# Kernel optimization log

Measured on AMD Instinct MI355X. Metric: run time of the kernel, lower is better.

Reference implementation:

```python
import jax, jax.numpy as jnp
import numpy as np
from jax import lax

K, D = 7, 2                      # kernel_size, dilation
PAD = (K - 1) * D                # = 12, matches init padding
B, CIN, COUT, L = 8, 128, 256, 4096


def _na_indices(L2, k, d):
    """NATTEN-style dilated 1D neighborhood: key positions + rel-pos-bias indices."""
    i = jnp.arange(L2)
    r, ii = i % d, i // d
    Lg = (L2 - r + d - 1) // d                       # dilation-group lengths
    start = jnp.clip(ii - k // 2, 0, Lg - k)         # clamped window start (in-group)
    t = jnp.arange(k)
    pos = r[:, None] + d * (start[:, None] + t[None, :])        # [L2,k] key positions
    bidx = start[:, None] + t[None, :] - ii[:, None] + (k - 1)  # [L2,k] rpb index in [0,2k-2]
    return pos, bidx


def setup_inputs() -> dict:
    key = jax.random.key(0)
    ks = jax.random.split(key, 11)
    s = 0.05
    return {
        "x": jax.random.normal(ks[0], (B, CIN, L), jnp.float32),
        "conv1_v": jax.random.normal(ks[1], (COUT, CIN, K), jnp.float32) * s,
        "conv1_g": jax.random.uniform(ks[2], (COUT,), jnp.float32, 0.5, 1.5),
        "conv1_b": jax.random.normal(ks[3], (COUT,), jnp.float32) * s,
        "qkv_w": jax.random.normal(ks[4], (3 * COUT, COUT), jnp.float32) * s,
        "qkv_b": jax.random.normal(ks[5], (3 * COUT,), jnp.float32) * s,
        "rpb": jax.random.normal(ks[6], (1, 2 * K - 1), jnp.float32) * s,
        "proj_w": jax.random.normal(ks[7], (COUT, COUT), jnp.float32) * s,
        "proj_b": jax.random.normal(ks[8], (COUT,), jnp.float32) * s,
        "ds_w": jax.random.normal(ks[9], (COUT, CIN, 1), jnp.float32) * s,
        "ds_b": jax.random.normal(ks[10], (COUT,), jnp.float32) * s,
    }


def reference(x, conv1_v, conv1_g, conv1_b, qkv_w, qkv_b, rpb, proj_w, proj_b, ds_w, ds_b):
    # weight_norm: w = g * v / ||v|| over (in_ch, kernel) per out channel
    vn = jnp.sqrt(jnp.sum(conv1_v * conv1_v, axis=(1, 2), keepdims=True))
    w1 = conv1_g[:, None, None] * conv1_v / vn
    out = lax.conv_general_dilated(x, w1, (1,), [(PAD, PAD)], rhs_dilation=(D,),
                                   dimension_numbers=("NCH", "OIH", "NCH"))
    out = out + conv1_b[None, :, None]
    out = jax.nn.relu(out[:, :, :-PAD])              # chomp1 + relu (dropout = eval identity)

    # left-pad then neighborhood attention on [B, L2, C]
    h = jnp.pad(out, ((0, 0), (0, 0), (PAD, 0))).transpose(0, 2, 1)
    L2 = h.shape[1]
    qkv = h @ qkv_w.T + qkv_b
    q, k_, v = jnp.split(qkv, 3, axis=-1)            # single head, head_dim = COUT
    pos, bidx = _na_indices(L2, K, D)
    kg = k_[:, pos, :]                               # [B, L2, K, C]
    vg = v[:, pos, :]
    scores = jnp.einsum("blc,blkc->blk", q * (COUT ** -0.5), kg) + rpb[0][bidx][None]
    attn = jax.nn.softmax(scores, axis=-1)
    o = jnp.einsum("blk,blkc->blc", attn, vg) @ proj_w.T + proj_b

    out = jax.nn.relu(o.transpose(0, 2, 1)[:, :, :-PAD])   # chomp2 + relu
    res = jnp.einsum("bcl,oc->bol", x, ds_w[:, :, 0]) + ds_b[None, :, None]
    return jax.nn.relu(out + res)
```

## Files before the change

### kernel.cpp

```cpp
#include <hip/hip_runtime.h>
#include <math.h>

#define KW 7
#define PADW 12
#define BATCH 8
#define CIN 128
#define COUT 256
#define LEN 4096
#define L2V 4108
#define NQKV 768
#define KCONV 896
#define PTILE 64

typedef unsigned short u16;
typedef short v8s __attribute__((ext_vector_type(8)));
typedef float v4f __attribute__((ext_vector_type(4)));

#define KEY3(r) ((((r) & 3) ^ (((r) >> 2) & 1)))

__device__ __forceinline__ u16 f2bf(float f) {
  unsigned int x = __float_as_uint(f);
  x += 0x7fffu + ((x >> 16) & 1u);
  return (u16)(x >> 16);
}
__device__ __forceinline__ float bf2f(u16 u) {
  return __uint_as_float(((unsigned int)u) << 16);
}

__device__ __forceinline__ void gll16(const void* g, void* l) {
  __builtin_amdgcn_global_load_lds(
      (const __attribute__((address_space(1))) void*)g,
      (__attribute__((address_space(3))) void*)l, 16, 0, 0);
}

#define MFMA8(ACC, AA, BB)                                                     \
  { _Pragma("unroll") for (int fi_ = 0; fi_ < 4; ++fi_)                        \
    _Pragma("unroll") for (int fj_ = 0; fj_ < 2; ++fj_)                        \
      ACC[fi_][fj_] = __builtin_amdgcn_mfma_f32_16x16x32_bf16(                 \
          AA[fi_], BB[fj_], ACC[fi_][fj_], 0, 0, 0); }

__global__ __launch_bounds__(256) void prep_wn(
    const float* __restrict__ v, const float* __restrict__ g,
    u16* __restrict__ wt)
{
  const int c = blockIdx.x;
  const float* vo = v + (size_t)c * (CIN * KW);
  float s = 0.f;
  for (int i = threadIdx.x; i < CIN * KW; i += 256) { float t = vo[i]; s += t * t; }
#pragma unroll
  for (int off = 1; off < 64; off <<= 1) s += __shfl_xor(s, off);
  __shared__ float red[4];
  if ((threadIdx.x & 63) == 0) red[threadIdx.x >> 6] = s;
  __syncthreads();
  const float tot = red[0] + red[1] + red[2] + red[3];
  const float scale = g[c] / sqrtf(tot);
  for (int i = threadIdx.x; i < CIN * KW; i += 256) {
    const int ci = i / 7, t = i - ci * 7;
    wt[((size_t)c * KW + t) * CIN + ci] = f2bf(vo[i] * scale);
  }
}

__global__ __launch_bounds__(256) void prep_cast(
    const float* __restrict__ qw, const float* __restrict__ pw,
    const float* __restrict__ dw, u16* __restrict__ qwb,
    u16* __restrict__ pwb, u16* __restrict__ dwb)
{
  const int i4 = (blockIdx.x * 256 + threadIdx.x) * 4;
  const float* src; u16* dst; int off;
  if (i4 < 196608)      { src = qw; dst = qwb; off = i4; }
  else if (i4 < 262144) { src = pw; dst = pwb; off = i4 - 196608; }
  else                  { src = dw; dst = dwb; off = i4 - 262144; }
  const float4 vv = *(const float4*)(src + off);
  *(ushort4*)(dst + off) = make_ushort4(f2bf(vv.x), f2bf(vv.y), f2bf(vv.z), f2bf(vv.w));
}

__global__ __launch_bounds__(256) void zero_fill(
    u16* __restrict__ xT, u16* __restrict__ qkv, const float* __restrict__ qb)
{
  const int idx = blockIdx.x * 256 + threadIdx.x;
  if (idx < BATCH * PADW * CIN) {
    const int b = idx / (PADW * CIN), r = idx - b * (PADW * CIN);
    xT[(size_t)b * L2V * CIN + r] = 0;
  } else {
    const int k = idx - BATCH * PADW * CIN;
    const int b = k / (PADW * NQKV), r2 = k - b * (PADW * NQKV);
    const int row = r2 / NQKV, n = r2 - row * NQKV;
    qkv[((size_t)b * L2V + row) * NQKV + n] = f2bf(qb[n]);
  }
}

__global__ __launch_bounds__(256) void xpose(const float* __restrict__ x, u16* __restrict__ xT)
{
  const int b = blockIdx.y, p0 = blockIdx.x * 64;
  const int tx = threadIdx.x & 15, ty = threadIdx.x >> 4;
  const int p = p0 + ty * 4;
  const float* xb = x + (size_t)b * CIN * LEN;
  u16* xTb = xT + (size_t)b * L2V * CIN + (size_t)(PADW + p) * CIN;
#pragma unroll
  for (int half = 0; half < 2; ++half) {
    const int ci0 = half * 64 + tx * 4;
    float r[4][4];
#pragma unroll
    for (int i = 0; i < 4; ++i)
      *(float4*)r[i] = *(const float4*)(xb + (size_t)(ci0 + i) * LEN + p);
#pragma unroll
    for (int j = 0; j < 4; ++j)
      *(ushort4*)(xTb + (size_t)j * CIN + ci0) =
          make_ushort4(f2bf(r[0][j]), f2bf(r[1][j]), f2bf(r[2][j]), f2bf(r[3][j]));
  }
}

__global__ __launch_bounds__(512, 4) void conv_qkv_fused(
    const u16* __restrict__ wt, const u16* __restrict__ xT,
    const float* __restrict__ c1b, const u16* __restrict__ qwb,
    const float* __restrict__ qb, u16* __restrict__ qkv)
{
  const int b = blockIdx.y;
  const int p0 = blockIdx.x * PTILE;
  const int tid = threadIdx.x;
  const int w = tid >> 6, lane = tid & 63;
  const int l15 = lane & 15, kg = lane >> 4;
  const int wA = w >> 1, wB = w & 1;

  __shared__ u16 hA[PTILE * 256];
  __shared__ u16 sA[2][256 * 32];
  __shared__ u16 sB[2][PTILE * 32];

  const u16* xTb = xT + (size_t)b * L2V * CIN + (size_t)p0 * CIN;

  v4f acc[4][2];
#pragma unroll
  for (int i = 0; i < 4; ++i)
#pragma unroll
    for (int j = 0; j < 2; ++j) acc[i][j] = (v4f){0.f, 0.f, 0.f, 0.f};

  auto stage_conv = [&](int s, int buf) {
    const int t = s >> 2, ci0 = (s & 3) << 5;
#pragma unroll
    for (int i = 0; i < 2; ++i) {
      const int cidx = i * 512 + tid;
      const int row = cidx >> 2, ch = cidx & 3;
      gll16(wt + (size_t)row * KCONV + t * CIN + ci0 + ((ch ^ KEY3(row)) << 3),
            (void*)&sA[buf][cidx * 8]);
    }
    if (tid < 256) {
      const int row = tid >> 2, ch = tid & 3;
      gll16(xTb + (size_t)(2 * t + row) * CIN + ci0 + ((ch ^ KEY3(row)) << 3),
            (void*)&sB[buf][tid * 8]);
    }
  };

  stage_conv(0, 0);
  __syncthreads();
  for (int s = 0; s < 28; ++s) {
    const int buf = s & 1;
    if (s < 27) stage_conv(s + 1, buf ^ 1);
    v8s a[4], bb[2];
#pragma unroll
    for (int f = 0; f < 4; ++f) {
      const int c = wA * 64 + f * 16 + l15;
      a[f] = *(const v8s*)&sA[buf][c * 32 + ((kg ^ KEY3(c)) << 3)];
    }
#pragma unroll
    for (int f = 0; f < 2; ++f) {
      const int p = wB * 32 + f * 16 + l15;
      bb[f] = *(const v8s*)&sB[buf][p * 32 + ((kg ^ KEY3(p)) << 3)];
    }
    MFMA8(acc, a, bb)
    __syncthreads();
  }

#pragma unroll
  for (int fi = 0; fi < 4; ++fi) {
    const int cb = wA * 64 + fi * 16 + kg * 4;
    const float4 bv = *(const float4*)(c1b + cb);
    const int ch32 = cb >> 3, off = cb & 7;
#pragma unroll
    for (int fj = 0; fj < 2; ++fj) {
      const int p = wB * 32 + fj * 16 + l15;
      *(ushort4*)&hA[p * 256 + ((ch32 ^ (p & 7)) << 3) + off] = make_ushort4(
          f2bf(fmaxf(acc[fi][fj][0] + bv.x, 0.f)),
          f2bf(fmaxf(acc[fi][fj][1] + bv.y, 0.f)),
          f2bf(fmaxf(acc[fi][fj][2] + bv.z, 0.f)),
          f2bf(fmaxf(acc[fi][fj][3] + bv.w, 0.f)));
      acc[fi][fj] = (v4f){0.f, 0.f, 0.f, 0.f};
    }
  }

  auto stage_qkv = [&](int st, int s, int buf) {
#pragma unroll
    for (int i = 0; i < 2; ++i) {
      const int cidx = i * 512 + tid;
      const int row = cidx >> 2, ch = cidx & 3;
      gll16(qwb + (size_t)(st * 256 + row) * COUT + (s << 5) + ((ch ^ KEY3(row)) << 3),
            (void*)&sA[buf][cidx * 8]);
    }
  };

  const size_t mg0 = (size_t)b * L2V + PADW + p0;
  for (int st = 0; st < 3; ++st) {
    stage_qkv(st, 0, 0);
    __syncthreads();
    for (int s = 0; s < 8; ++s) {
      const int buf = s & 1;
      if (s < 7) stage_qkv(st, s + 1, buf ^ 1);
      v8s a[4], bb[2];
#pragma unroll
      for (int f = 0; f < 4; ++f) {
        const int n = wA * 64 + f * 16 + l15;
        a[f] = *(const v8s*)&sA[buf][n * 32 + ((kg ^ KEY3(n)) << 3)];
      }
#pragma unroll
      for (int f = 0; f < 2; ++f) {
        const int m = wB * 32 + f * 16 + l15;
        bb[f] = *(const v8s*)&hA[m * 256 + ((((s << 2) + kg) ^ (m & 7)) << 3)];
      }
      MFMA8(acc, a, bb)
      __syncthreads();
    }
    u16* T = &sA[0][0];
#pragma unroll
    for (int h2 = 0; h2 < 2; ++h2) {
#pragma unroll
      for (int f1 = 0; f1 < 2; ++f1) {
        const int fi = 2 * h2 + f1;
        const int j = wA * 32 + f1 * 16 + kg * 4;
        const int jc8 = j >> 3, noff = j & 7;
        const float4 bv = *(const float4*)(qb + st * 256 + wA * 64 + h2 * 32 + f1 * 16 + kg * 4);
#pragma unroll
        for (int fj = 0; fj < 2; ++fj) {
          const int m = wB * 32 + fj * 16 + l15;
          *(ushort4*)&T[m * 128 + ((jc8 ^ (m & 15)) << 3) + noff] = make_ushort4(
              f2bf(acc[fi][fj][0] + bv.x), f2bf(acc[fi][fj][1] + bv.y),
              f2bf(acc[fi][fj][2] + bv.z), f2bf(acc[fi][fj][3] + bv.w));
          acc[fi][fj] = (v4f){0.f, 0.f, 0.f, 0.f};
        }
      }
      __syncthreads();
#pragma unroll
      for (int i2 = 0; i2 < 2; ++i2) {
        const int cidx = i2 * 512 + tid;
        const int m = cidx >> 4, j16 = cidx & 15;
        const int4 vv = *(const int4*)&T[m * 128 + ((j16 ^ (m & 15)) << 3)];
        const int n = (j16 >> 2) * 64 + h2 * 32 + (j16 & 3) * 8;
        *(int4*)(qkv + (mg0 + m) * NQKV + st * 256 + n) = vv;
      }
      __syncthreads();
    }
  }
}

__global__ __launch_bounds__(256) void attn_bf16(
    const u16* __restrict__ qkv, const float* __restrict__ rpb,
    u16* __restrict__ ao)
{
  const int wid = (blockIdx.x << 2) + (threadIdx.x >> 6);
  const int lane = threadIdx.x & 63;
  const int b = wid >> 12;
  const int j = wid & 4095;
  const int r = j & 1, ii = j >> 1;
  int start = ii - 3;
  start = start < 0 ? 0 : start;
  start = start > 2047 ? 2047 : start;

  const u16* base = qkv + (size_t)b * L2V * NQKV;
  const ushort4 qv = *(const ushort4*)(base + (size_t)j * NQKV + 4 * lane);
  const float q0 = bf2f(qv.x) * 0.0625f, q1 = bf2f(qv.y) * 0.0625f;
  const float q2 = bf2f(qv.z) * 0.0625f, q3 = bf2f(qv.w) * 0.0625f;

  float sc[7];
  float mx = -1e30f;
#pragma unroll
  for (int t = 0; t < 7; ++t) {
    const int pos = r + 2 * (start + t);
    const ushort4 kv = *(const ushort4*)(base + (size_t)pos * NQKV + COUT + 4 * lane);
    float s = q0 * bf2f(kv.x) + q1 * bf2f(kv.y) + q2 * bf2f(kv.z) + q3 * bf2f(kv.w);
#pragma unroll
    for (int o = 1; o < 64; o <<= 1) s += __shfl_xor(s, o);
    s += rpb[start + t - ii + 6];
    sc[t] = s;
    mx = fmaxf(mx, s);
  }
  float sum = 0.f;
#pragma unroll
  for (int t = 0; t < 7; ++t) { sc[t] = __expf(sc[t] - mx); sum += sc[t]; }
  const float inv = 1.f / sum;

  float a0 = 0.f, a1 = 0.f, a2 = 0.f, a3 = 0.f;
#pragma unroll
  for (int t = 0; t < 7; ++t) {
    const int pos = r + 2 * (start + t);
    const ushort4 vv = *(const ushort4*)(base + (size_t)pos * NQKV + 2 * COUT + 4 * lane);
    const float wgt = sc[t] * inv;
    a0 += wgt * bf2f(vv.x); a1 += wgt * bf2f(vv.y);
    a2 += wgt * bf2f(vv.z); a3 += wgt * bf2f(vv.w);
  }
  *(ushort4*)(ao + ((size_t)(b * LEN + j)) * COUT + 4 * lane) =
      make_ushort4(f2bf(a0), f2bf(a1), f2bf(a2), f2bf(a3));
}

__global__ __launch_bounds__(256, 2) void projds_gll(
    const u16* __restrict__ ao, const u16* __restrict__ pwb,
    const float* __restrict__ pb, const u16* __restrict__ xT,
    const u16* __restrict__ dwb, const float* __restrict__ db,
    float* __restrict__ out)
{
  const int b = blockIdx.z;
  const int l0 = blockIdx.x * 128, o0 = blockIdx.y * 128;
  const int tid = threadIdx.x;
  const int w = tid >> 6, lane = tid & 63;
  const int l15 = lane & 15, kg = lane >> 4;
  const int wr = w >> 1, wc = w & 1;

  __shared__ u16 sX[2][128 * 32];
  __shared__ u16 sW[2][128 * 32];

  const int arow = tid >> 2, ach = tid & 3;
  const int akey = KEY3(arow);
  const u16* aob = ao + (size_t)b * LEN * COUT;
  const u16* xTb = xT + ((size_t)b * L2V + PADW) * CIN;

  auto stage1 = [&](int s, int buf) {
#pragma unroll
    for (int i = 0; i < 2; ++i) {
      const int row = i * 64 + arow;
      const int sl = (ach ^ akey) << 3;
      gll16(aob + (size_t)(l0 + row) * COUT + (s << 5) + sl,
            (void*)&sX[buf][(i * 256 + tid) * 8]);
      gll16(pwb + (size_t)(o0 + row) * COUT + (s << 5) + sl,
            (void*)&sW[buf][(i * 256 + tid) * 8]);
    }
  };
  auto stage2 = [&](int s, int buf) {
#pragma unroll
    for (int i = 0; i < 2; ++i) {
      const int row = i * 64 + arow;
      const int sl = (ach ^ akey) << 3;
      gll16(xTb + (size_t)(l0 + row) * CIN + (s << 5) + sl,
            (void*)&sX[buf][(i * 256 + tid) * 8]);
      gll16(dwb + (size_t)(o0 + row) * CIN + (s << 5) + sl,
            (void*)&sW[buf][(i * 256 + tid) * 8]);
    }
  };

  v4f acc[4][4];
#pragma unroll
  for (int i = 0; i < 4; ++i)
#pragma unroll
    for (int j = 0; j < 4; ++j) acc[i][j] = (v4f){0.f, 0.f, 0.f, 0.f};

  stage1(0, 0);
  __syncthreads();
  for (int ss = 0; ss < 12; ++ss) {
    const int buf = ss & 1;
    if (ss < 7) stage1(ss + 1, buf ^ 1);
    else if (ss < 11) stage2(ss - 7, buf ^ 1);
    v8s a[4], bb[4];
#pragma unroll
    for (int f = 0; f < 4; ++f) {
      const int lr = wr * 64 + f * 16 + l15;
      a[f] = *(const v8s*)&sX[buf][lr * 32 + ((kg ^ KEY3(lr)) << 3)];
      const int orr = wc * 64 + f * 16 + l15;
      bb[f] = *(const v8s*)&sW[buf][orr * 32 + ((kg ^ KEY3(orr)) << 3)];
    }
#pragma unroll
    for (int fi_ = 0; fi_ < 4; ++fi_)
#pragma unroll
      for (int fj_ = 0; fj_ < 4; ++fj_)
        acc[fi_][fj_] = __builtin_amdgcn_mfma_f32_16x16x32_bf16(
            a[fi_], bb[fj_], acc[fi_][fj_], 0, 0, 0);
    if (ss == 7) {
#pragma unroll
      for (int fj = 0; fj < 4; ++fj) {
        const float pbv = pb[o0 + wc * 64 + fj * 16 + l15];
#pragma unroll
        for (int fi = 0; fi < 4; ++fi)
#pragma unroll
          for (int jj = 0; jj < 4; ++jj)
            acc[fi][fj][jj] = fmaxf(acc[fi][fj][jj] + pbv, 0.f);
      }
    }
    __syncthreads();
  }

#pragma unroll
  for (int fj = 0; fj < 4; ++fj) {
    const int o = o0 + wc * 64 + fj * 16 + l15;
    const float dbv = db[o];
    float* orow = out + ((size_t)(b * COUT + o)) * LEN;
#pragma unroll
    for (int fi = 0; fi < 4; ++fi) {
      const int lb = l0 + wr * 64 + fi * 16 + kg * 4;
      float v0 = acc[fi][fj][0] + dbv; v0 = v0 > 0.f ? v0 : 0.f;
      float v1 = acc[fi][fj][1] + dbv; v1 = v1 > 0.f ? v1 : 0.f;
      float v2 = acc[fi][fj][2] + dbv; v2 = v2 > 0.f ? v2 : 0.f;
      float v3 = acc[fi][fj][3] + dbv; v3 = v3 > 0.f ? v3 : 0.f;
      *(float4*)(orow + lb) = make_float4(v0, v1, v2, v3);
    }
  }
}

extern "C" void kernel_launch(void* const* d_in, const int* in_sizes, int n_in,
                              void* d_out, int out_size, void* d_ws, size_t ws_size,
                              hipStream_t stream)
{
  (void)in_sizes; (void)n_in; (void)out_size; (void)ws_size;
  const float* x   = (const float*)d_in[0];
  const float* c1v = (const float*)d_in[1];
  const float* c1g = (const float*)d_in[2];
  const float* c1b = (const float*)d_in[3];
  const float* qw  = (const float*)d_in[4];
  const float* qb  = (const float*)d_in[5];
  const float* rpb = (const float*)d_in[6];
  const float* pw  = (const float*)d_in[7];
  const float* pb  = (const float*)d_in[8];
  const float* dw  = (const float*)d_in[9];
  const float* db  = (const float*)d_in[10];
  float* out = (float*)d_out;

  char* ws = (char*)d_ws;
  u16* wt  = (u16*)(ws);
  u16* qwb = (u16*)(ws + 458752);
  u16* pwb = (u16*)(ws + 851968);
  u16* dwb = (u16*)(ws + 983040);
  u16* xT  = (u16*)(ws + 1048576);
  u16* qkv = (u16*)(ws + 26288128);
  u16* ao  = (u16*)(ws + 76767232);

  prep_wn<<<COUT, 256, 0, stream>>>(c1v, c1g, wt);
  prep_cast<<<288, 256, 0, stream>>>(qw, pw, dw, qwb, pwb, dwb);
  zero_fill<<<336, 256, 0, stream>>>(xT, qkv, qb);
  xpose<<<dim3(LEN / 64, BATCH), 256, 0, stream>>>(x, xT);
  conv_qkv_fused<<<dim3(LEN / PTILE, BATCH), 512, 0, stream>>>(wt, xT, c1b, qwb, qb, qkv);
  attn_bf16<<<(BATCH * LEN) / 4, 256, 0, stream>>>(qkv, rpb, ao);
  projds_gll<<<dim3(LEN / 128, COUT / 128, BATCH), 256, 0, stream>>>(ao, pwb, pb, xT, dwb, db, out);
}
```

Baseline: 103.1 us.

## Load QKV weight fragments directly to registers and pad h tile stride

```diff
diff --git a/kernel.cpp b/kernel.cpp
--- a/kernel.cpp
+++ b/kernel.cpp
@@ -11,6 +11,7 @@
 #define NQKV 768
 #define KCONV 896
 #define PTILE 64
+#define HSTR 272
 
 typedef unsigned short u16;
 typedef short v8s __attribute__((ext_vector_type(8)));
@@ -122,7 +123,7 @@
   const int l15 = lane & 15, kg = lane >> 4;
   const int wA = w >> 1, wB = w & 1;
 
-  __shared__ u16 hA[PTILE * 256];
+  __shared__ u16 hA[PTILE * HSTR];
   __shared__ u16 sA[2][256 * 32];
   __shared__ u16 sB[2][PTILE * 32];
 
@@ -174,11 +175,10 @@
   for (int fi = 0; fi < 4; ++fi) {
     const int cb = wA * 64 + fi * 16 + kg * 4;
     const float4 bv = *(const float4*)(c1b + cb);
-    const int ch32 = cb >> 3, off = cb & 7;
 #pragma unroll
     for (int fj = 0; fj < 2; ++fj) {
       const int p = wB * 32 + fj * 16 + l15;
-      *(ushort4*)&hA[p * 256 + ((ch32 ^ (p & 7)) << 3) + off] = make_ushort4(
+      *(ushort4*)&hA[p * HSTR + cb] = make_ushort4(
           f2bf(fmaxf(acc[fi][fj][0] + bv.x, 0.f)),
           f2bf(fmaxf(acc[fi][fj][1] + bv.y, 0.f)),
           f2bf(fmaxf(acc[fi][fj][2] + bv.z, 0.f)),
@@ -186,39 +186,48 @@
       acc[fi][fj] = (v4f){0.f, 0.f, 0.f, 0.f};
     }
   }
-
-  auto stage_qkv = [&](int st, int s, int buf) {
-#pragma unroll
-    for (int i = 0; i < 2; ++i) {
-      const int cidx = i * 512 + tid;
-      const int row = cidx >> 2, ch = cidx & 3;
-      gll16(qwb + (size_t)(st * 256 + row) * COUT + (s << 5) + ((ch ^ KEY3(row)) << 3),
-            (void*)&sA[buf][cidx * 8]);
-    }
-  };
+  __syncthreads();
 
   const size_t mg0 = (size_t)b * L2V + PADW + p0;
+  u16* T = &sA[0][0];
+
+  v8s A0[4], A1[4];
+#pragma unroll
+  for (int f = 0; f < 4; ++f) {
+    const u16* basep = qwb + (size_t)(wA * 64 + f * 16 + l15) * COUT + kg * 8;
+    A0[f] = *(const v8s*)(basep);
+    A1[f] = *(const v8s*)(basep + 32);
+  }
+
+#pragma unroll
   for (int st = 0; st < 3; ++st) {
-    stage_qkv(st, 0, 0);
-    __syncthreads();
+#pragma unroll
     for (int s = 0; s < 8; ++s) {
-      const int buf = s & 1;
-      if (s < 7) stage_qkv(st, s + 1, buf ^ 1);
-      v8s a[4], bb[2];
-#pragma unroll
-      for (int f = 0; f < 4; ++f) {
-        const int n = wA * 64 + f * 16 + l15;
-        a[f] = *(const v8s*)&sA[buf][n * 32 + ((kg ^ KEY3(n)) << 3)];
-      }
+      v8s bb[2];
 #pragma unroll
       for (int f = 0; f < 2; ++f) {
         const int m = wB * 32 + f * 16 + l15;
-        bb[f] = *(const v8s*)&hA[m * 256 + ((((s << 2) + kg) ^ (m & 7)) << 3)];
-      }
-      MFMA8(acc, a, bb)
-      __syncthreads();
-    }
-    u16* T = &sA[0][0];
+        bb[f] = *(const v8s*)&hA[m * HSTR + s * 32 + kg * 8];
+      }
+      if (s & 1) { MFMA8(acc, A1, bb) } else { MFMA8(acc, A0, bb) }
+      if (s < 6) {
+#pragma unroll
+        for (int f = 0; f < 4; ++f) {
+          const u16* basep = qwb +
+              (size_t)(st * 256 + wA * 64 + f * 16 + l15) * COUT + (s + 2) * 32 + kg * 8;
+          if (s & 1) A1[f] = *(const v8s*)basep; else A0[f] = *(const v8s*)basep;
+        }
+      }
+    }
+    if (st < 2) {
+#pragma unroll
+      for (int f = 0; f < 4; ++f) {
+        const u16* basep = qwb +
+            (size_t)((st + 1) * 256 + wA * 64 + f * 16 + l15) * COUT + kg * 8;
+        A0[f] = *(const v8s*)(basep);
+        A1[f] = *(const v8s*)(basep + 32);
+      }
+    }
 #pragma unroll
     for (int h2 = 0; h2 < 2; ++h2) {
 #pragma unroll
```

Result: slower. 130.0 us (+26.1%).

## Double tile width and triple-buffer conv/QKV GEMM with explicit vmcnt waits

Applied to the files above, without the earlier changes.

```diff
diff --git a/kernel.cpp b/kernel.cpp
--- a/kernel.cpp
+++ b/kernel.cpp
@@ -10,7 +10,7 @@
 #define L2V 4108
 #define NQKV 768
 #define KCONV 896
-#define PTILE 64
+#define PTILE 128
 
 typedef unsigned short u16;
 typedef short v8s __attribute__((ext_vector_type(8)));
@@ -33,9 +33,20 @@
       (__attribute__((address_space(3))) void*)l, 16, 0, 0);
 }
 
-#define MFMA8(ACC, AA, BB)                                                     \
+__device__ __forceinline__ void wait_vm(int n) {
+  switch (n) {
+    case 0:  asm volatile("s_waitcnt vmcnt(0)" ::: "memory"); break;
+    case 2:  asm volatile("s_waitcnt vmcnt(2)" ::: "memory"); break;
+    case 3:  asm volatile("s_waitcnt vmcnt(3)" ::: "memory"); break;
+    case 10: asm volatile("s_waitcnt vmcnt(10)" ::: "memory"); break;
+  }
+}
+#define LGKM0()  asm volatile("s_waitcnt lgkmcnt(0)" ::: "memory")
+#define BARRIER() { __builtin_amdgcn_s_barrier(); asm volatile("" ::: "memory"); }
+
+#define MFMA16(ACC, AA, BB)                                                    \
   { _Pragma("unroll") for (int fi_ = 0; fi_ < 4; ++fi_)                        \
-    _Pragma("unroll") for (int fj_ = 0; fj_ < 2; ++fj_)                        \
+    _Pragma("unroll") for (int fj_ = 0; fj_ < 4; ++fj_)                        \
       ACC[fi_][fj_] = __builtin_amdgcn_mfma_f32_16x16x32_bf16(                 \
           AA[fi_], BB[fj_], ACC[fi_][fj_], 0, 0, 0); }
 
@@ -110,7 +121,7 @@
   }
 }
 
-__global__ __launch_bounds__(512, 4) void conv_qkv_fused(
+__global__ __launch_bounds__(512, 2) void conv_qkv_fused(
     const u16* __restrict__ wt, const u16* __restrict__ xT,
     const float* __restrict__ c1b, const u16* __restrict__ qwb,
     const float* __restrict__ qb, u16* __restrict__ qkv)
@@ -123,51 +134,52 @@
   const int wA = w >> 1, wB = w & 1;
 
   __shared__ u16 hA[PTILE * 256];
-  __shared__ u16 sA[2][256 * 32];
-  __shared__ u16 sB[2][PTILE * 32];
+  __shared__ u16 pool[40960];
 
   const u16* xTb = xT + (size_t)b * L2V * CIN + (size_t)p0 * CIN;
 
-  v4f acc[4][2];
+  v4f acc[4][4];
 #pragma unroll
   for (int i = 0; i < 4; ++i)
 #pragma unroll
-    for (int j = 0; j < 2; ++j) acc[i][j] = (v4f){0.f, 0.f, 0.f, 0.f};
-
-  auto stage_conv = [&](int s, int buf) {
+    for (int j = 0; j < 4; ++j) acc[i][j] = (v4f){0.f, 0.f, 0.f, 0.f};
+
+  auto stageA = [&](int s, int buf) {
     const int t = s >> 2, ci0 = (s & 3) << 5;
+    u16* dst = pool + buf * 12288;
 #pragma unroll
     for (int i = 0; i < 2; ++i) {
       const int cidx = i * 512 + tid;
       const int row = cidx >> 2, ch = cidx & 3;
       gll16(wt + (size_t)row * KCONV + t * CIN + ci0 + ((ch ^ KEY3(row)) << 3),
-            (void*)&sA[buf][cidx * 8]);
-    }
-    if (tid < 256) {
+            (void*)(dst + cidx * 8));
+    }
+    {
       const int row = tid >> 2, ch = tid & 3;
       gll16(xTb + (size_t)(2 * t + row) * CIN + ci0 + ((ch ^ KEY3(row)) << 3),
-            (void*)&sB[buf][tid * 8]);
+            (void*)(dst + 8192 + tid * 8));
     }
   };
 
-  stage_conv(0, 0);
-  __syncthreads();
+  stageA(0, 0);
+  stageA(1, 1);
+
+#pragma unroll
   for (int s = 0; s < 28; ++s) {
-    const int buf = s & 1;
-    if (s < 27) stage_conv(s + 1, buf ^ 1);
-    v8s a[4], bb[2];
+    if (s < 27) wait_vm(3); else wait_vm(0);
+    BARRIER()
+    if (s < 26) stageA(s + 2, (s + 2) % 3);
+    const u16* wbuf = pool + (s % 3) * 12288;
+    const u16* xbuf = wbuf + 8192;
+    v8s a[4], bb[4];
 #pragma unroll
     for (int f = 0; f < 4; ++f) {
       const int c = wA * 64 + f * 16 + l15;
-      a[f] = *(const v8s*)&sA[buf][c * 32 + ((kg ^ KEY3(c)) << 3)];
-    }
-#pragma unroll
-    for (int f = 0; f < 2; ++f) {
-      const int p = wB * 32 + f * 16 + l15;
-      bb[f] = *(const v8s*)&sB[buf][p * 32 + ((kg ^ KEY3(p)) << 3)];
-    }
-    MFMA8(acc, a, bb)
-    __syncthreads();
+      a[f] = *(const v8s*)&wbuf[c * 32 + ((kg ^ KEY3(c)) << 3)];
+      const int p = wB * 64 + f * 16 + l15;
+      bb[f] = *(const v8s*)&xbuf[p * 32 + ((kg ^ KEY3(p)) << 3)];
+    }
+    MFMA16(acc, a, bb)
   }
 
 #pragma unroll
@@ -176,8 +188,8 @@
     const float4 bv = *(const float4*)(c1b + cb);
     const int ch32 = cb >> 3, off = cb & 7;
 #pragma unroll
-    for (int fj = 0; fj < 2; ++fj) {
-      const int p = wB * 32 + fj * 16 + l15;
+    for (int fj = 0; fj < 4; ++fj) {
+      const int p = wB * 64 + fj * 16 + l15;
       *(ushort4*)&hA[p * 256 + ((ch32 ^ (p & 7)) << 3) + off] = make_ushort4(
           f2bf(fmaxf(acc[fi][fj][0] + bv.x, 0.f)),
           f2bf(fmaxf(acc[fi][fj][1] + bv.y, 0.f)),
@@ -186,66 +198,79 @@
       acc[fi][fj] = (v4f){0.f, 0.f, 0.f, 0.f};
     }
   }
-
-  auto stage_qkv = [&](int st, int s, int buf) {
+  LGKM0();
+  BARRIER()
+
+  auto stageB = [&](int it2, int buf) {
+    const int nt = it2 >> 3, k0 = (it2 & 7) << 5;
+    u16* dst = pool + buf * 8192;
 #pragma unroll
     for (int i = 0; i < 2; ++i) {
       const int cidx = i * 512 + tid;
       const int row = cidx >> 2, ch = cidx & 3;
-      gll16(qwb + (size_t)(st * 256 + row) * COUT + (s << 5) + ((ch ^ KEY3(row)) << 3),
-            (void*)&sA[buf][cidx * 8]);
+      gll16(qwb + (size_t)(nt * 256 + row) * COUT + k0 + ((ch ^ KEY3(row)) << 3),
+            (void*)(dst + cidx * 8));
     }
   };
+  stageB(0, 0);
+  stageB(1, 1);
 
   const size_t mg0 = (size_t)b * L2V + PADW + p0;
-  for (int st = 0; st < 3; ++st) {
-    stage_qkv(st, 0, 0);
-    __syncthreads();
-    for (int s = 0; s < 8; ++s) {
-      const int buf = s & 1;
-      if (s < 7) stage_qkv(st, s + 1, buf ^ 1);
-      v8s a[4], bb[2];
-#pragma unroll
-      for (int f = 0; f < 4; ++f) {
-        const int n = wA * 64 + f * 16 + l15;
-        a[f] = *(const v8s*)&sA[buf][n * 32 + ((kg ^ KEY3(n)) << 3)];
+  u16* T = pool + 24576;
+
+#pragma unroll
+  for (int it = 0; it < 24; ++it) {
+    const int s = it & 7, st = it >> 3;
+    if (it == 23) wait_vm(0);
+    else if (it >= 8 && s <= 1) wait_vm(10);
+    else wait_vm(2);
+    BARRIER()
+    if (it < 22) stageB(it + 2, (it + 2) % 3);
+    const u16* nbuf = pool + (it % 3) * 8192;
+    v8s a[4], bb[4];
+#pragma unroll
+    for (int f = 0; f < 4; ++f) {
+      const int n = wA * 64 + f * 16 + l15;
+      a[f] = *(const v8s*)&nbuf[n * 32 + ((kg ^ KEY3(n)) << 3)];
+      const int m = wB * 64 + f * 16 + l15;
+      bb[f] = *(const v8s*)&hA[m * 256 + ((((s << 2) + kg) ^ (m & 7)) << 3)];
+    }
+    MFMA16(acc, a, bb)
+
+    if (s == 7) {
+#pragma unroll
+      for (int h2 = 0; h2 < 2; ++h2) {
+        if ((wA >> 1) == h2) {
+#pragma unroll
+          for (int fi = 0; fi < 4; ++fi) {
+            const int j = (wA & 1) * 64 + fi * 16 + kg * 4;
+            const float4 bv = *(const float4*)(qb + st * 256 + h2 * 128 + j);
+            const int jc = j >> 3, joff = j & 7;
+#pragma unroll
+            for (int fj = 0; fj < 4; ++fj) {
+              const int m = wB * 64 + fj * 16 + l15;
+              *(ushort4*)&T[m * 128 + ((jc ^ (m & 15)) << 3) + joff] = make_ushort4(
+                  f2bf(acc[fi][fj][0] + bv.x), f2bf(acc[fi][fj][1] + bv.y),
+                  f2bf(acc[fi][fj][2] + bv.z), f2bf(acc[fi][fj][3] + bv.w));
+            }
+          }
+        }
+        LGKM0();
+        BARRIER()
+#pragma unroll
+        for (int i2 = 0; i2 < 4; ++i2) {
+          const int chunk = i2 * 512 + tid;
+          const int m = chunk >> 4, j16 = chunk & 15;
+          const int4 vv = *(const int4*)&T[m * 128 + ((j16 ^ (m & 15)) << 3)];
+          *(int4*)(qkv + (mg0 + m) * NQKV + st * 256 + h2 * 128 + j16 * 8) = vv;
+        }
+        LGKM0();
+        BARRIER()
       }
 #pragma unroll
-      for (int f = 0; f < 2; ++f) {
-        const int m = wB * 32 + f * 16 + l15;
-        bb[f] = *(const v8s*)&hA[m * 256 + ((((s << 2) + kg) ^ (m & 7)) << 3)];
-      }
-      MFMA8(acc, a, bb)
-      __syncthreads();
-    }
-    u16* T = &sA[0][0];
-#pragma unroll
-    for (int h2 = 0; h2 < 2; ++h2) {
-#pragma unroll
-      for (int f1 = 0; f1 < 2; ++f1) {
-        const int fi = 2 * h2 + f1;
-        const int j = wA * 32 + f1 * 16 + kg * 4;
-        const int jc8 = j >> 3, noff = j & 7;
-        const float4 bv = *(const float4*)(qb + st * 256 + wA * 64 + h2 * 32 + f1 * 16 + kg * 4);
-#pragma unroll
-        for (int fj = 0; fj < 2; ++fj) {
-          const int m = wB * 32 + fj * 16 + l15;
-          *(ushort4*)&T[m * 128 + ((jc8 ^ (m & 15)) << 3) + noff] = make_ushort4(
-              f2bf(acc[fi][fj][0] + bv.x), f2bf(acc[fi][fj][1] + bv.y),
-              f2bf(acc[fi][fj][2] + bv.z), f2bf(acc[fi][fj][3] + bv.w));
-          acc[fi][fj] = (v4f){0.f, 0.f, 0.f, 0.f};
-        }
-      }
-      __syncthreads();
-#pragma unroll
-      for (int i2 = 0; i2 < 2; ++i2) {
-        const int cidx = i2 * 512 + tid;
-        const int m = cidx >> 4, j16 = cidx & 15;
-        const int4 vv = *(const int4*)&T[m * 128 + ((j16 ^ (m & 15)) << 3)];
-        const int n = (j16 >> 2) * 64 + h2 * 32 + (j16 & 3) * 8;
-        *(int4*)(qkv + (mg0 + m) * NQKV + st * 256 + n) = vv;
-      }
-      __syncthreads();
+      for (int fi = 0; fi < 4; ++fi)
+#pragma unroll
+        for (int fj = 0; fj < 4; ++fj) acc[fi][fj] = (v4f){0.f, 0.f, 0.f, 0.f};
     }
   }
 }
```

Result: slower. 106.1 us (+2.9%).
